# Performance work log

Measured on AMD Instinct MI355X. Metric: run time of the kernel, lower is better.

The kernel has to match this reference:

```python
import jax, jax.numpy as jnp
import numpy as np

N_NODES = 80000
N_EDGES = 1280000
D_NODE = 128
D_EDGE = 32
D_HID = 64
NEG_SLOPE = 0.2


def setup_inputs() -> dict:
    key = jax.random.key(0)
    ks = jax.random.split(key, 9)
    return {
        "node_features": jax.random.normal(ks[0], (N_NODES, D_NODE), dtype=jnp.float32),
        "edge_features": jax.random.normal(ks[1], (N_EDGES, D_EDGE), dtype=jnp.float32),
        "edge_index": jax.random.randint(ks[2], (2, N_EDGES), 0, N_NODES, dtype=jnp.int64),
        # params: w (node Linear), edgew (edge Linear), attn (3*hid -> 1)
        "w_w": jax.random.normal(ks[3], (D_NODE, D_HID), dtype=jnp.float32) / np.sqrt(D_NODE),
        "w_b": jax.random.normal(ks[4], (D_HID,), dtype=jnp.float32) * 0.01,
        "ew_w": jax.random.normal(ks[5], (D_EDGE, D_HID), dtype=jnp.float32) / np.sqrt(D_EDGE),
        "ew_b": jax.random.normal(ks[6], (D_HID,), dtype=jnp.float32) * 0.01,
        "a_w": jax.random.normal(ks[7], (3 * D_HID, 1), dtype=jnp.float32) / np.sqrt(3 * D_HID),
        "a_b": jax.random.normal(ks[8], (1,), dtype=jnp.float32) * 0.01,
    }


def reference(node_features, edge_features, edge_index, w_w, w_b, ew_w, ew_b, a_w, a_b):
    n_nodes = node_features.shape[0]
    h = node_features @ w_w + w_b              # [N, H]
    edge_h = edge_features @ ew_w + ew_b       # [E, H]
    tgt = edge_index[0]                        # target (softmax group) nodes i
    nbr = edge_index[1]                        # neighbor nodes j
    h_i = h[tgt]                               # [E, H] gather
    h_j = h[nbr]                               # [E, H] gather
    h_concat = jnp.concatenate([h_i, h_j, edge_h], axis=-1)  # [E, 3H]
    eij = jax.nn.leaky_relu(h_concat @ a_w + a_b, negative_slope=NEG_SLOPE)  # [E, 1]
    # scatter-softmax over edges grouped by target node (numerically stable)
    seg_max = jax.ops.segment_max(eij, tgt, num_segments=n_nodes)            # [N, 1]
    ex = jnp.exp(eij - seg_max[tgt])
    seg_sum = jax.ops.segment_sum(ex, tgt, num_segments=n_nodes)             # [N, 1]
    alpha = ex / seg_sum[tgt]                                                # [E, 1]
    # (dropout omitted for deterministic reference)
    message = alpha * h_j                                                    # [E, H]
    out = jax.ops.segment_sum(message, tgt, num_segments=n_nodes)            # [N, H]
    return jax.nn.elu(out)
```

## Files before the change

### kernel.cpp

```cpp
#include <hip/hip_runtime.h>
#include <math.h>

#define N_NODES 80000
#define N_EDGES 1280000
#define D_NODE  128
#define D_EDGE  32
#define D_HID   64
#define NEG_SLOPE 0.2f
#define NB 313
#define CAP 4608
#define BCNT_STRIDE 16
#define EB_BLK 512
#define EB_CHUNK 2048
#define EB_NCHUNK (N_EDGES / EB_CHUNK)

__device__ inline float waveReduceSum(float v) {
    #pragma unroll
    for (int o = 32; o > 0; o >>= 1) v += __shfl_xor(v, o);
    return v;
}
__device__ inline unsigned short f2bf(float f) {
    unsigned u = __float_as_uint(f);
    return (unsigned short)((u + 0x7FFF + ((u >> 16) & 1)) >> 16);
}
__device__ inline float bf2f(unsigned short v) {
    return __uint_as_float(((unsigned)v) << 16);
}

__global__ __launch_bounds__(256) void node_kernel(
        const float* __restrict__ nf, const float* __restrict__ w_w,
        const float* __restrict__ w_b, const float* __restrict__ a_w,
        unsigned short* __restrict__ hb, float* __restrict__ s1, float* __restrict__ s2) {
    __shared__ float Ws[D_HID * D_NODE];
    __shared__ float Xs[32][D_NODE];
    for (int i = threadIdx.x; i < D_NODE * D_HID; i += 256) {
        int k = i >> 6, d = i & 63;
        Ws[d * D_NODE + (((k >> 2) ^ (d & 7)) << 2) + (k & 3)] = w_w[i];
    }
    int lane = threadIdx.x & 63;
    int wv   = threadIdx.x >> 6;
    float wb = w_b[lane];
    float a1 = a_w[lane];
    float a2 = a_w[D_HID + lane];
    const float* wrow = &Ws[lane * D_NODE];
    const int nTiles = N_NODES / 32;
    for (int tile = blockIdx.x; tile < nTiles; tile += gridDim.x) {
        int n0 = tile * 32;
        __syncthreads();
        {
            const float4* src = (const float4*)(nf + (size_t)n0 * D_NODE);
            float4* dst = (float4*)&Xs[0][0];
            #pragma unroll
            for (int j = 0; j < 4; ++j)
                dst[threadIdx.x + 256 * j] = src[threadIdx.x + 256 * j];
        }
        __syncthreads();
        float acc[8] = {0.f, 0.f, 0.f, 0.f, 0.f, 0.f, 0.f, 0.f};
        const float* xs = &Xs[wv * 8][0];
        #pragma unroll 4
        for (int k4 = 0; k4 < 32; ++k4) {
            float4 w = *(const float4*)&wrow[(k4 ^ (lane & 7)) << 2];
            #pragma unroll
            for (int n = 0; n < 8; ++n) {
                float4 x = *(const float4*)&xs[n * D_NODE + (k4 << 2)];
                acc[n] += w.x * x.x + w.y * x.y + w.z * x.z + w.w * x.w;
            }
        }
        #pragma unroll
        for (int n = 0; n < 8; ++n) {
            int node = n0 + wv * 8 + n;
            float hv = acc[n] + wb;
            hb[(size_t)node * D_HID + lane] = f2bf(hv);
            float r1 = waveReduceSum(hv * a1);
            float r2 = waveReduceSum(hv * a2);
            if (lane == 0) { s1[node] = r1; s2[node] = r2; }
        }
    }
}

__global__ __launch_bounds__(EB_BLK) void edge_bin_kernel(
        const float* __restrict__ ef, const int* __restrict__ eidx,
        const float* __restrict__ s2v,
        const float* __restrict__ ew_w, const float* __restrict__ ew_b,
        const float* __restrict__ a_w, const float* __restrict__ a_b,
        int* __restrict__ bcnt, int2* __restrict__ binned) {
    __shared__ float cs[D_EDGE];
    __shared__ float bes;
    __shared__ int hist[NB], gbase[NB], rank[NB];
    __shared__ float sq [EB_CHUNK];
    __shared__ int   stg[EB_CHUNK];
    __shared__ int   snb[EB_CHUNK];
    int tid = threadIdx.x;
    if (tid < D_EDGE) {
        float s = 0.f;
        #pragma unroll
        for (int d = 0; d < D_HID; ++d) s += ew_w[tid * D_HID + d] * a_w[2 * D_HID + d];
        cs[tid] = s;
    } else if (tid == D_EDGE) {
        float s = 0.f;
        #pragma unroll
        for (int d = 0; d < D_HID; ++d) s += ew_b[d] * a_w[2 * D_HID + d];
        bes = s + a_b[0];
    }
    int qd = tid >> 2;
    int j  = tid & 3;
    for (int c = blockIdx.x; c < EB_NCHUNK; c += gridDim.x) {
        for (int i = tid; i < NB; i += EB_BLK) { hist[i] = 0; rank[i] = 0; }
        __syncthreads();
        int e0 = c * EB_CHUNK;
        #pragma unroll
        for (int k = 0; k < 4; ++k) {
            int idx = k * EB_BLK + tid;
            int e = e0 + idx;
            int tg = eidx[e];
            int nb = eidx[N_EDGES + e];
            stg[idx] = tg;
            snb[idx] = nb;
            sq [idx] = bes + s2v[nb];
            atomicAdd(&hist[tg >> 8], 1);
        }
        __syncthreads();
        #pragma unroll 2
        for (int rr = 0; rr < EB_CHUNK / 128; ++rr) {
            int idx = rr * 128 + qd;
            int e = e0 + idx;
            const float4* f4 = (const float4*)ef;
            float4 fa = f4[(size_t)e * 8 + j];
            float4 fb = f4[(size_t)e * 8 + 4 + j];
            const float4 c1 = *(const float4*)&cs[j * 4];
            const float4 c2 = *(const float4*)&cs[16 + j * 4];
            float p = fa.x * c1.x + fa.y * c1.y + fa.z * c1.z + fa.w * c1.w
                    + fb.x * c2.x + fb.y * c2.y + fb.z * c2.z + fb.w * c2.w;
            p += __shfl_xor(p, 1);
            p += __shfl_xor(p, 2);
            if (j == 0) sq[idx] += p;
        }
        __syncthreads();
        for (int i = tid; i < NB; i += EB_BLK) {
            int cc = hist[i];
            if (cc) gbase[i] = i * CAP + atomicAdd(&bcnt[i * BCNT_STRIDE], cc);
        }
        __syncthreads();
        #pragma unroll
        for (int k = 0; k < 4; ++k) {
            int idx = k * EB_BLK + tid;
            int tg = stg[idx];
            int b  = tg >> 8;
            int r  = atomicAdd(&rank[b], 1);
            binned[gbase[b] + r] = make_int2(((tg & 255) << 17) | snb[idx],
                                             __float_as_int(sq[idx]));
        }
        __syncthreads();
    }
}

__global__ __launch_bounds__(512) void bucket_scan_kernel(
        const int* __restrict__ bcnt, int* __restrict__ bbase,
        int* __restrict__ node_off) {
    __shared__ int buf[512];
    int v = (threadIdx.x < NB) ? bcnt[threadIdx.x * BCNT_STRIDE] : 0;
    buf[threadIdx.x] = v;
    __syncthreads();
    for (int ofs = 1; ofs < 512; ofs <<= 1) {
        int t = (threadIdx.x >= (unsigned)ofs) ? buf[threadIdx.x - ofs] : 0;
        __syncthreads();
        buf[threadIdx.x] += t;
        __syncthreads();
    }
    if (threadIdx.x < NB) bbase[threadIdx.x] = buf[threadIdx.x] - v;
    if (threadIdx.x == NB - 1) bbase[NB] = buf[threadIdx.x];
    if (threadIdx.x == 0) node_off[N_NODES] = N_EDGES;
}

__global__ __launch_bounds__(256) void bucket_csr_kernel(
        const int* __restrict__ bcnt, const int* __restrict__ bbase,
        const int2* __restrict__ binned, int* __restrict__ node_off,
        int2* __restrict__ pay2) {
    __shared__ int nhist[256], buf[256], ncur[256];
    int b = blockIdx.x;
    int in0  = b * CAP;
    int cnt  = bcnt[b * BCNT_STRIDE];
    int out0 = bbase[b];
    nhist[threadIdx.x] = 0;
    __syncthreads();
    for (int i = threadIdx.x; i < cnt; i += 256)
        atomicAdd(&nhist[binned[in0 + i].x >> 17], 1);
    __syncthreads();
    int v = nhist[threadIdx.x];
    buf[threadIdx.x] = v;
    __syncthreads();
    for (int ofs = 1; ofs < 256; ofs <<= 1) {
        int t = (threadIdx.x >= (unsigned)ofs) ? buf[threadIdx.x - ofs] : 0;
        __syncthreads();
        buf[threadIdx.x] += t;
        __syncthreads();
    }
    int excl = buf[threadIdx.x] - v;
    int n = b * 256 + (int)threadIdx.x;
    if (n < N_NODES) node_off[n] = out0 + excl;
    ncur[threadIdx.x] = excl;
    __syncthreads();
    for (int i = threadIdx.x; i < cnt; i += 256) {
        int2 p = binned[in0 + i];
        int r = atomicAdd(&ncur[p.x >> 17], 1);
        pay2[out0 + r] = make_int2(p.x & 0x1FFFF, p.y);
    }
}

__global__ __launch_bounds__(256) void accum_kernel(
        const int* __restrict__ node_off, const int2* __restrict__ pay2,
        const float* __restrict__ s1, const unsigned short* __restrict__ hb,
        float* __restrict__ out) {
    int tid = threadIdx.x;
    int wv = tid >> 6, lane = tid & 63;
    int grp = lane >> 4, li = lane & 15;
    int node = blockIdx.x * 16 + wv * 4 + grp;
    int base = node_off[node];
    int cnt  = node_off[node + 1] - base;
    float s1i = s1[node];
    float ax = 0.f, ay = 0.f, az = 0.f, aw = 0.f;
    float sumex = 0.f;
    for (int c0 = 0; c0 < cnt; c0 += 16) {
        int i = c0 + li;
        int nc = min(16, cnt - c0);
        float exv = 0.f; int nbv = 0;
        if (i < cnt) {
            int2 p = pay2[base + i];
            nbv = p.x;
            float s = s1i + __int_as_float(p.y);
            s = (s > 0.f) ? s : NEG_SLOPE * s;
            exv = __expf(s);
        }
        sumex += exv;
        for (int j = 0; j < nc; ++j) {
            float w  = __shfl(exv, grp * 16 + j);
            int   nb = __shfl(nbv, grp * 16 + j);
            uint2 v = *(const uint2*)&hb[(size_t)nb * D_HID + li * 4];
            ax += w * bf2f((unsigned short)(v.x & 0xFFFF));
            ay += w * bf2f((unsigned short)(v.x >> 16));
            az += w * bf2f((unsigned short)(v.y & 0xFFFF));
            aw += w * bf2f((unsigned short)(v.y >> 16));
        }
    }
    #pragma unroll
    for (int o = 8; o > 0; o >>= 1) sumex += __shfl_xor(sumex, o);
    float4 o4;
    if (cnt == 0) {
        o4 = make_float4(0.f, 0.f, 0.f, 0.f);
    } else {
        o4.x = ax / sumex; o4.y = ay / sumex; o4.z = az / sumex; o4.w = aw / sumex;
        o4.x = (o4.x > 0.f) ? o4.x : (__expf(o4.x) - 1.f);
        o4.y = (o4.y > 0.f) ? o4.y : (__expf(o4.y) - 1.f);
        o4.z = (o4.z > 0.f) ? o4.z : (__expf(o4.z) - 1.f);
        o4.w = (o4.w > 0.f) ? o4.w : (__expf(o4.w) - 1.f);
    }
    ((float4*)out)[(size_t)node * 16 + li] = o4;
}

extern "C" void kernel_launch(void* const* d_in, const int* in_sizes, int n_in,
                              void* d_out, int out_size, void* d_ws, size_t ws_size,
                              hipStream_t stream) {
    const float* nf   = (const float*)d_in[0];
    const float* ef   = (const float*)d_in[1];
    const int*   eidx = (const int*)d_in[2];
    const float* w_w  = (const float*)d_in[3];
    const float* w_b  = (const float*)d_in[4];
    const float* ew_w = (const float*)d_in[5];
    const float* ew_b = (const float*)d_in[6];
    const float* a_w  = (const float*)d_in[7];
    const float* a_b  = (const float*)d_in[8];
    float* out = (float*)d_out;

    char* ws = (char*)d_ws;
    size_t o = 0;
    auto alloc = [&](size_t bytes) -> void* {
        void* p = ws + o;
        o = (o + bytes + 255) & ~(size_t)255;
        return p;
    };
    unsigned short* hb  = (unsigned short*)alloc((size_t)N_NODES * D_HID * 2);
    float* s1       = (float*)alloc((size_t)N_NODES * 4);
    float* s2       = (float*)alloc((size_t)N_NODES * 4);
    int*   bcnt     = (int*)alloc((size_t)NB * BCNT_STRIDE * 4);
    int*   bbase    = (int*)alloc((size_t)(NB + 1) * 4);
    int*   node_off = (int*)alloc((size_t)(N_NODES + 1) * 4);
    int2*  binned   = (int2*)alloc((size_t)NB * CAP * 8);
    int2*  pay2     = (int2*)alloc((size_t)N_EDGES * 8);

    hipMemsetAsync(bcnt, 0, (size_t)NB * BCNT_STRIDE * 4, stream);

    node_kernel<<<1250, 256, 0, stream>>>(nf, w_w, w_b, a_w, hb, s1, s2);
    edge_bin_kernel<<<EB_NCHUNK, EB_BLK, 0, stream>>>(ef, eidx, s2, ew_w, ew_b, a_w, a_b, bcnt, binned);
    bucket_scan_kernel<<<1, 512, 0, stream>>>(bcnt, bbase, node_off);
    bucket_csr_kernel<<<NB, 256, 0, stream>>>(bcnt, bbase, binned, node_off, pay2);
    accum_kernel<<<N_NODES / 16, 256, 0, stream>>>(node_off, pay2, s1, hb, out);
}
```

Measured before the change: 156.5 us.

## Fuse bucket scan, CSR build and accumulation into one per-bucket kernel

Replaces the bucket scan, CSR scatter and accumulate kernels with one kernel per bucket. Each bucket's edges are sorted by node into a shared-memory slab and then aggregated in the same block, so the global pay2 and node_off round trips and two launches go away. The trade-off is only 313 blocks of 1024 threads with a large shared-memory slab (CAP*8 bytes), which lowers occupancy and the parallelism available to the gather-heavy accumulation phase.

After: 149.2 us. 4.7% less time.

```diff
diff --git a/kernel.cpp b/kernel.cpp
--- a/kernel.cpp
+++ b/kernel.cpp
@@ -154,107 +154,88 @@
     }
 }
 
-__global__ __launch_bounds__(512) void bucket_scan_kernel(
-        const int* __restrict__ bcnt, int* __restrict__ bbase,
-        int* __restrict__ node_off) {
-    __shared__ int buf[512];
-    int v = (threadIdx.x < NB) ? bcnt[threadIdx.x * BCNT_STRIDE] : 0;
-    buf[threadIdx.x] = v;
-    __syncthreads();
-    for (int ofs = 1; ofs < 512; ofs <<= 1) {
-        int t = (threadIdx.x >= (unsigned)ofs) ? buf[threadIdx.x - ofs] : 0;
-        __syncthreads();
-        buf[threadIdx.x] += t;
-        __syncthreads();
-    }
-    if (threadIdx.x < NB) bbase[threadIdx.x] = buf[threadIdx.x] - v;
-    if (threadIdx.x == NB - 1) bbase[NB] = buf[threadIdx.x];
-    if (threadIdx.x == 0) node_off[N_NODES] = N_EDGES;
-}
-
-__global__ __launch_bounds__(256) void bucket_csr_kernel(
-        const int* __restrict__ bcnt, const int* __restrict__ bbase,
-        const int2* __restrict__ binned, int* __restrict__ node_off,
-        int2* __restrict__ pay2) {
-    __shared__ int nhist[256], buf[256], ncur[256];
+__global__ __launch_bounds__(1024) void bucket_accum_kernel(
+        const int* __restrict__ bcnt, const int2* __restrict__ binned,
+        const float* __restrict__ s1, const unsigned short* __restrict__ hb,
+        float* __restrict__ out) {
+    __shared__ int nhist[256], buf[256], sbase[256], ncur[256];
+    __shared__ int2 slab[CAP];
+    int tid = threadIdx.x;
     int b = blockIdx.x;
-    int in0  = b * CAP;
-    int cnt  = bcnt[b * BCNT_STRIDE];
-    int out0 = bbase[b];
-    nhist[threadIdx.x] = 0;
-    __syncthreads();
-    for (int i = threadIdx.x; i < cnt; i += 256)
+    int in0 = b * CAP;
+    int cnt = bcnt[b * BCNT_STRIDE];
+    if (tid < 256) nhist[tid] = 0;
+    __syncthreads();
+    for (int i = tid; i < cnt; i += 1024)
         atomicAdd(&nhist[binned[in0 + i].x >> 17], 1);
     __syncthreads();
-    int v = nhist[threadIdx.x];
-    buf[threadIdx.x] = v;
+    if (tid < 256) buf[tid] = nhist[tid];
     __syncthreads();
     for (int ofs = 1; ofs < 256; ofs <<= 1) {
-        int t = (threadIdx.x >= (unsigned)ofs) ? buf[threadIdx.x - ofs] : 0;
-        __syncthreads();
-        buf[threadIdx.x] += t;
-        __syncthreads();
-    }
-    int excl = buf[threadIdx.x] - v;
-    int n = b * 256 + (int)threadIdx.x;
-    if (n < N_NODES) node_off[n] = out0 + excl;
-    ncur[threadIdx.x] = excl;
-    __syncthreads();
-    for (int i = threadIdx.x; i < cnt; i += 256) {
+        int t = 0;
+        if (tid < 256 && tid >= ofs) t = buf[tid - ofs];
+        __syncthreads();
+        if (tid < 256) buf[tid] += t;
+        __syncthreads();
+    }
+    if (tid < 256) {
+        int excl = buf[tid] - nhist[tid];
+        sbase[tid] = excl;
+        ncur[tid]  = excl;
+    }
+    __syncthreads();
+    for (int i = tid; i < cnt; i += 1024) {
         int2 p = binned[in0 + i];
         int r = atomicAdd(&ncur[p.x >> 17], 1);
-        pay2[out0 + r] = make_int2(p.x & 0x1FFFF, p.y);
-    }
-}
-
-__global__ __launch_bounds__(256) void accum_kernel(
-        const int* __restrict__ node_off, const int2* __restrict__ pay2,
-        const float* __restrict__ s1, const unsigned short* __restrict__ hb,
-        float* __restrict__ out) {
-    int tid = threadIdx.x;
-    int wv = tid >> 6, lane = tid & 63;
-    int grp = lane >> 4, li = lane & 15;
-    int node = blockIdx.x * 16 + wv * 4 + grp;
-    int base = node_off[node];
-    int cnt  = node_off[node + 1] - base;
-    float s1i = s1[node];
-    float ax = 0.f, ay = 0.f, az = 0.f, aw = 0.f;
-    float sumex = 0.f;
-    for (int c0 = 0; c0 < cnt; c0 += 16) {
-        int i = c0 + li;
-        int nc = min(16, cnt - c0);
-        float exv = 0.f; int nbv = 0;
-        if (i < cnt) {
-            int2 p = pay2[base + i];
-            nbv = p.x;
-            float s = s1i + __int_as_float(p.y);
-            s = (s > 0.f) ? s : NEG_SLOPE * s;
-            exv = __expf(s);
-        }
-        sumex += exv;
-        for (int j = 0; j < nc; ++j) {
-            float w  = __shfl(exv, grp * 16 + j);
-            int   nb = __shfl(nbv, grp * 16 + j);
-            uint2 v = *(const uint2*)&hb[(size_t)nb * D_HID + li * 4];
-            ax += w * bf2f((unsigned short)(v.x & 0xFFFF));
-            ay += w * bf2f((unsigned short)(v.x >> 16));
-            az += w * bf2f((unsigned short)(v.y & 0xFFFF));
-            aw += w * bf2f((unsigned short)(v.y >> 16));
-        }
-    }
-    #pragma unroll
-    for (int o = 8; o > 0; o >>= 1) sumex += __shfl_xor(sumex, o);
-    float4 o4;
-    if (cnt == 0) {
-        o4 = make_float4(0.f, 0.f, 0.f, 0.f);
-    } else {
-        o4.x = ax / sumex; o4.y = ay / sumex; o4.z = az / sumex; o4.w = aw / sumex;
-        o4.x = (o4.x > 0.f) ? o4.x : (__expf(o4.x) - 1.f);
-        o4.y = (o4.y > 0.f) ? o4.y : (__expf(o4.y) - 1.f);
-        o4.z = (o4.z > 0.f) ? o4.z : (__expf(o4.z) - 1.f);
-        o4.w = (o4.w > 0.f) ? o4.w : (__expf(o4.w) - 1.f);
-    }
-    ((float4*)out)[(size_t)node * 16 + li] = o4;
+        slab[r] = make_int2(p.x & 0x1FFFF, p.y);
+    }
+    __syncthreads();
+    int grp = tid >> 4;
+    int li  = tid & 15;
+    int wl  = ((tid & 63) >> 4) << 4;
+    for (int nl = grp; nl < 256; nl += 64) {
+        int node = b * 256 + nl;
+        if (node >= N_NODES) break;
+        int base = sbase[nl];
+        int cn   = nhist[nl];
+        float s1i = s1[node];
+        float ax = 0.f, ay = 0.f, az = 0.f, aw = 0.f, sumex = 0.f;
+        for (int c0 = 0; c0 < cn; c0 += 16) {
+            int i = c0 + li;
+            int nc = min(16, cn - c0);
+            float exv = 0.f; int nbv = 0;
+            if (i < cn) {
+                int2 p = slab[base + i];
+                nbv = p.x;
+                float s = s1i + __int_as_float(p.y);
+                s = (s > 0.f) ? s : NEG_SLOPE * s;
+                exv = __expf(s);
+            }
+            sumex += exv;
+            for (int j = 0; j < nc; ++j) {
+                float w  = __shfl(exv, wl + j);
+                int   nb = __shfl(nbv, wl + j);
+                uint2 v = *(const uint2*)&hb[(size_t)nb * D_HID + li * 4];
+                ax += w * bf2f((unsigned short)(v.x & 0xFFFF));
+                ay += w * bf2f((unsigned short)(v.x >> 16));
+                az += w * bf2f((unsigned short)(v.y & 0xFFFF));
+                aw += w * bf2f((unsigned short)(v.y >> 16));
+            }
+        }
+        #pragma unroll
+        for (int o = 8; o > 0; o >>= 1) sumex += __shfl_xor(sumex, o);
+        float4 o4;
+        if (cn == 0) {
+            o4 = make_float4(0.f, 0.f, 0.f, 0.f);
+        } else {
+            o4.x = ax / sumex; o4.y = ay / sumex; o4.z = az / sumex; o4.w = aw / sumex;
+            o4.x = (o4.x > 0.f) ? o4.x : (__expf(o4.x) - 1.f);
+            o4.y = (o4.y > 0.f) ? o4.y : (__expf(o4.y) - 1.f);
+            o4.z = (o4.z > 0.f) ? o4.z : (__expf(o4.z) - 1.f);
+            o4.w = (o4.w > 0.f) ? o4.w : (__expf(o4.w) - 1.f);
+        }
+        ((float4*)out)[(size_t)node * 16 + li] = o4;
+    }
 }
 
 extern "C" void kernel_launch(void* const* d_in, const int* in_sizes, int n_in,
@@ -282,16 +263,11 @@
     float* s1       = (float*)alloc((size_t)N_NODES * 4);
     float* s2       = (float*)alloc((size_t)N_NODES * 4);
     int*   bcnt     = (int*)alloc((size_t)NB * BCNT_STRIDE * 4);
-    int*   bbase    = (int*)alloc((size_t)(NB + 1) * 4);
-    int*   node_off = (int*)alloc((size_t)(N_NODES + 1) * 4);
     int2*  binned   = (int2*)alloc((size_t)NB * CAP * 8);
-    int2*  pay2     = (int2*)alloc((size_t)N_EDGES * 8);
 
     hipMemsetAsync(bcnt, 0, (size_t)NB * BCNT_STRIDE * 4, stream);
 
     node_kernel<<<1250, 256, 0, stream>>>(nf, w_w, w_b, a_w, hb, s1, s2);
     edge_bin_kernel<<<EB_NCHUNK, EB_BLK, 0, stream>>>(ef, eidx, s2, ew_w, ew_b, a_w, a_b, bcnt, binned);
-    bucket_scan_kernel<<<1, 512, 0, stream>>>(bcnt, bbase, node_off);
-    bucket_csr_kernel<<<NB, 256, 0, stream>>>(bcnt, bbase, binned, node_off, pay2);
-    accum_kernel<<<N_NODES / 16, 256, 0, stream>>>(node_off, pay2, s1, hb, out);
-}
+    bucket_accum_kernel<<<NB, 1024, 0, stream>>>(bcnt, binned, s1, hb, out);
+}
```
